# Optimization experiments

Hardware: AMD Instinct MI355X
Metric: run time of the kernel (lower is better)

## Reference

```python
import jax, jax.numpy as jnp
import numpy as np

N_HIDDEN = 15


def lstm_cell(x, h, c, W_ih, W_hh, b_ih, b_hh):
    # x: [B, in], h/c: [B, H]. PyTorch LSTMCell gate order: i, f, g, o
    gates = x @ W_ih.T + h @ W_hh.T + b_ih + b_hh  # [B, 4H]
    i, f, g, o = jnp.split(gates, 4, axis=-1)
    i = jax.nn.sigmoid(i)
    f = jax.nn.sigmoid(f)
    g = jnp.tanh(g)
    o = jax.nn.sigmoid(o)
    c_new = f * c + i * g
    h_new = o * jnp.tanh(c_new)
    return h_new, c_new


def setup_inputs() -> dict:
    key = jax.random.key(0)
    ks = jax.random.split(key, 12)
    B, T, H = 4096, 1024, N_HIDDEN
    s = 1.0 / np.sqrt(H)  # torch default init bound
    u = lambda k, shape: jax.random.uniform(k, shape, jnp.float32, -s, s)
    return {
        "input": jax.random.normal(ks[0], (B, T), jnp.float32),
        "W_ih1": u(ks[1], (4 * H, 1)),
        "W_hh1": u(ks[2], (4 * H, H)),
        "b_ih1": u(ks[3], (4 * H,)),
        "b_hh1": u(ks[4], (4 * H,)),
        "W_ih2": u(ks[5], (4 * H, H)),
        "W_hh2": u(ks[6], (4 * H, H)),
        "b_ih2": u(ks[7], (4 * H,)),
        "b_hh2": u(ks[8], (4 * H,)),
        "W_lin": u(ks[9], (1, H)),
        "b_lin": u(ks[10], (1,)),
        "future": 64,
    }


def reference(input, W_ih1, W_hh1, b_ih1, b_hh1, W_ih2, W_hh2, b_ih2, b_hh2, W_lin, b_lin, future):
    B = input.shape[0]
    H = N_HIDDEN
    zeros = jnp.zeros((B, H), input.dtype)

    def step(carry, x_t):
        h1, c1, h2, c2 = carry
        h1, c1 = lstm_cell(x_t, h1, c1, W_ih1, W_hh1, b_ih1, b_hh1)
        h2, c2 = lstm_cell(h1, h2, c2, W_ih2, W_hh2, b_ih2, b_hh2)
        out = h2 @ W_lin.T + b_lin  # [B, 1]
        return (h1, c1, h2, c2), out

    xs = input.T[:, :, None]  # [T, B, 1]
    carry, outs = jax.lax.scan(step, (zeros, zeros, zeros, zeros), xs)

    last_out = outs[-1]  # [B, 1]

    def fut_step(carry, _):
        h1, c1, h2, c2, out = carry
        (h1, c1, h2, c2), out = step((h1, c1, h2, c2), out)
        return (h1, c1, h2, c2, out), out

    _, fut_outs = jax.lax.scan(fut_step, (*carry, last_out), None, length=future)

    all_outs = jnp.concatenate([outs, fut_outs], axis=0)  # [T+future, B, 1]
    return all_outs[:, :, 0].T  # [B, T+future]
```

## Files before the change

### kernel.cpp

```cpp
#include <hip/hip_runtime.h>

#define HID   15
#define TMAIN 1024
#define FUT   64
#define OUTW  (TMAIN + FUT)

typedef _Float16 v2h __attribute__((ext_vector_type(2)));

__device__ __forceinline__ float rcp_(float x)  { return __builtin_amdgcn_rcpf(x); }
__device__ __forceinline__ float exp2_(float x) { return __builtin_amdgcn_exp2f(x); }
__device__ __forceinline__ float tanh_(float x) {
    return __builtin_fmaf(2.0f, rcp_(1.0f + exp2_(x * -2.885390081777927f)), -1.0f);
}

template<int I> struct ic { static constexpr int v = I; };
template<int J, int N, class F>
__device__ __forceinline__ void unroll_for(F&& f) {
    if constexpr (J < N) { f(ic<J>{}); unroll_for<J + 1, N>(f); }
}

template<int CTRL>
__device__ __forceinline__ int dppi(int x) {
    return __builtin_amdgcn_update_dpp(0, x, CTRL, 0xF, 0xF, true);
}
template<int CTRL>
__device__ __forceinline__ float dppf(float x) {
    return __int_as_float(dppi<CTRL>(__float_as_int(x)));
}
__device__ __forceinline__ float row_sum_bcast(float p) {
    p += dppf<0x111>(p);
    p += dppf<0x112>(p);
    p += dppf<0x114>(p);
    p += dppf<0x118>(p);
    return dppf<0x15F>(p);
}
__device__ __forceinline__ float fdot2(v2h a, v2h b, float c) {
    return __builtin_amdgcn_fdot2(a, b, c, false);
}
__device__ __forceinline__ v2h pkrtz(float lo, float hi) {
    return __builtin_bit_cast(v2h, __builtin_amdgcn_cvt_pkrtz(lo, hi));
}

__global__ __launch_bounds__(256)
__attribute__((amdgpu_waves_per_eu(1, 1)))
void lstm_seq_kernel(const float* __restrict__ input,
                     const float* __restrict__ W_ih1, const float* __restrict__ W_hh1,
                     const float* __restrict__ b_ih1, const float* __restrict__ b_hh1,
                     const float* __restrict__ W_ih2, const float* __restrict__ W_hh2,
                     const float* __restrict__ b_ih2, const float* __restrict__ b_hh2,
                     const float* __restrict__ W_lin, const float* __restrict__ b_lin,
                     float* __restrict__ out)
{
    const int tid  = threadIdx.x;
    const int wq   = tid >> 6;
    const int lane = tid & 63;
    const int g    = lane >> 4;
    const int k    = lane & 15;
    const int b0   = (blockIdx.x * 4 + wq) * 4;

    const bool pad = (k >= HID);
    const float m  = pad ? 0.0f : 1.0f;
    const int  kk  = pad ? 0 : k;

    const float L2E = 1.442695040888963f;
    const float sA[4] = {-L2E, -L2E, -2.0f * L2E, -L2E};

    v2h w1[4][8], w2i[4][8], w2h[4][8];
    float bb1[4], bb2[4];
    #pragma unroll
    for (int gi = 0; gi < 4; ++gi) {
        const int row = gi * HID + kk;
        const float s = m * sA[gi];
        bb1[gi] = s * (b_ih1[row] + b_hh1[row]);
        bb2[gi] = s * (b_ih2[row] + b_hh2[row]);
        #pragma unroll
        for (int j = 0; j < 8; ++j) {
            const int c0 = 2 * j, c1i = 2 * j + 1;
            w1 [gi][j] = (v2h){(_Float16)(s * W_hh1[row * HID + c0]),
                               (_Float16)((c1i < HID) ? s * W_hh1[row * HID + c1i]
                                                      : s * W_ih1[row])};
            w2i[gi][j] = (v2h){(_Float16)(s * W_ih2[row * HID + c0]),
                               (_Float16)((c1i < HID) ? s * W_ih2[row * HID + c1i] : 0.0f)};
            w2h[gi][j] = (v2h){(_Float16)(s * W_hh2[row * HID + c0]),
                               (_Float16)((c1i < HID) ? s * W_hh2[row * HID + c1i] : 0.0f)};
        }
    }
    const float wl   = m * W_lin[kk];
    const float blin = b_lin[0];

    auto packh = [&](float h) -> int {
        const _Float16 hh = (_Float16)h;
        const int lo = (int)(unsigned short)__builtin_bit_cast(unsigned short, hh);
        const int hi = dppi<0x101>(lo);
        const v2h pr = {__builtin_bit_cast(_Float16, (unsigned short)lo),
                        __builtin_bit_cast(_Float16, (unsigned short)(hi & 0xFFFF))};
        return __builtin_bit_cast(int, pr);
    };

    v2h hb1[8];
    #pragma unroll
    for (int j = 0; j < 8; ++j) hb1[j] = (v2h){(_Float16)0.0f, (_Float16)0.0f};
    int hpk2 = 0;
    float c1 = 0.0f, c2 = 0.0f, outv = 0.0f;

    auto step = [&](auto Sc, auto UseOvC, float xvpre, float& oreg) {
        constexpr int  S      = decltype(Sc)::v;
        constexpr bool USE_OV = decltype(UseOvC)::v;

        float a0 = bb1[0], a1 = bb1[1], a2 = bb1[2], a3 = bb1[3];
        unroll_for<0, 8>([&](auto jc) {
            constexpr int j = decltype(jc)::v;
            a0 = fdot2(w1[0][j], hb1[j], a0);
            a1 = fdot2(w1[1][j], hb1[j], a1);
            a2 = fdot2(w1[2][j], hb1[j], a2);
            a3 = fdot2(w1[3][j], hb1[j], a3);
        });

        float d0 = bb2[0], d1 = bb2[1], d2 = bb2[2], d3 = bb2[3];
        unroll_for<0, 8>([&](auto jc) {
            constexpr int j = decltype(jc)::v;
            const v2h hb = __builtin_bit_cast(v2h, dppi<0x150 + 2*j>(hpk2));
            d0 = fdot2(w2h[0][j], hb, d0);
            d1 = fdot2(w2h[1][j], hb, d1);
            d2 = fdot2(w2h[2][j], hb, d2);
            d3 = fdot2(w2h[3][j], hb, d3);
        });

        const float ig = rcp_(1.0f + exp2_(a0));
        const float fg = rcp_(1.0f + exp2_(a1));
        const float gg = __builtin_fmaf(2.0f, rcp_(1.0f + exp2_(a2)), -1.0f);
        const float og = rcp_(1.0f + exp2_(a3));
        c1 = __builtin_fmaf(fg, c1, ig * gg);
        const float h1n = og * tanh_(c1);

        const int hpk1 = packh(h1n);
        unroll_for<0, 8>([&](auto jc) {
            constexpr int j = decltype(jc)::v;
            hb1[j] = __builtin_bit_cast(v2h, dppi<0x150 + 2*j>(hpk1));
        });
        unroll_for<0, 8>([&](auto jc) {
            constexpr int j = decltype(jc)::v;
            d0 = fdot2(w2i[0][j], hb1[j], d0);
            d1 = fdot2(w2i[1][j], hb1[j], d1);
            d2 = fdot2(w2i[2][j], hb1[j], d2);
            d3 = fdot2(w2i[3][j], hb1[j], d3);
        });

        const float i2 = rcp_(1.0f + exp2_(d0));
        const float f2 = rcp_(1.0f + exp2_(d1));
        const float g2 = __builtin_fmaf(2.0f, rcp_(1.0f + exp2_(d2)), -1.0f);
        const float o2 = rcp_(1.0f + exp2_(d3));
        c2 = __builtin_fmaf(f2, c2, i2 * g2);
        const float h2n = o2 * tanh_(c2);
        hpk2 = packh(h2n);

        const float ov = row_sum_bcast(wl * h2n) + blin;
        oreg = (k == S) ? ov : oreg;

        const float xv = USE_OV ? ov : xvpre;
        hb1[7] = pkrtz(dppf<0x15E>(h1n), xv);

        outv = ov;
    };

    const size_t inb  = (size_t)(b0 + g) * TMAIN + k;
    const size_t outb = (size_t)(b0 + g) * OUTW  + k;

    float xcur = input[inb];
    hb1[7] = pkrtz(0.0f, dppf<0x150>(xcur));

    #pragma unroll 1
    for (int ch = 0; ch < TMAIN / 16; ++ch) {
        const bool last = (ch == TMAIN / 16 - 1);
        const float xnext = input[inb + (last ? ch : ch + 1) * 16];
        float oreg = 0.0f;
        unroll_for<0, 16>([&](auto sc) {
            constexpr int s = decltype(sc)::v;
            if constexpr (s < 15) {
                step(sc, ic<0>{}, dppf<0x150 + s + 1>(xcur), oreg);
            } else {
                if (last) step(sc, ic<1>{}, 0.0f, oreg);
                else      step(sc, ic<0>{}, dppf<0x150>(xnext), oreg);
            }
        });
        out[outb + ch * 16] = oreg;
        xcur = xnext;
    }

    #pragma unroll 1
    for (int ch = 0; ch < FUT / 16; ++ch) {
        float oreg = 0.0f;
        unroll_for<0, 16>([&](auto sc) {
            step(sc, ic<1>{}, 0.0f, oreg);
        });
        out[outb + TMAIN + ch * 16] = oreg;
    }
}

extern "C" void kernel_launch(void* const* d_in, const int* in_sizes, int n_in,
                              void* d_out, int out_size, void* d_ws, size_t ws_size,
                              hipStream_t stream)
{
    const float* input = (const float*)d_in[0];
    const float* W_ih1 = (const float*)d_in[1];
    const float* W_hh1 = (const float*)d_in[2];
    const float* b_ih1 = (const float*)d_in[3];
    const float* b_hh1 = (const float*)d_in[4];
    const float* W_ih2 = (const float*)d_in[5];
    const float* W_hh2 = (const float*)d_in[6];
    const float* b_ih2 = (const float*)d_in[7];
    const float* b_hh2 = (const float*)d_in[8];
    const float* W_lin = (const float*)d_in[9];
    const float* b_lin = (const float*)d_in[10];

    lstm_seq_kernel<<<256, 256, 0, stream>>>(
        input, W_ih1, W_hh1, b_ih1, b_hh1,
        W_ih2, W_hh2, b_ih2, b_hh2, W_lin, b_lin,
        (float*)d_out);
}
```

Measured before the change: 471.4 us.

## Replace per-lane fdot2 gate matvecs with MFMA 16x16x32 matrix ops

The recurrent and input gate matvecs, which were done with chains of v_dot2 instructions on DPP-broadcast hidden states, now run on MFMA 16x16x32 f16. Weights are packed into A operands with the bias folded in as an extra K column. The B operand is built from packed h via ds_bpermute, and results are redistributed to lanes with bpermute plus selects. The aim is to cut VALU dot-product work on the sequential critical path. In exchange each step pays MFMA latency and LDS-crossbar permutes, and most of the 16x16 output is wasted work.

```diff
diff --git a/kernel.cpp b/kernel.cpp
--- a/kernel.cpp
+++ b/kernel.cpp
@@ -6,6 +6,9 @@
 #define OUTW  (TMAIN + FUT)
 
 typedef _Float16 v2h __attribute__((ext_vector_type(2)));
+typedef _Float16 v8h __attribute__((ext_vector_type(8)));
+typedef float    v4f __attribute__((ext_vector_type(4)));
+typedef int      v4i __attribute__((ext_vector_type(4)));
 
 __device__ __forceinline__ float rcp_(float x)  { return __builtin_amdgcn_rcpf(x); }
 __device__ __forceinline__ float exp2_(float x) { return __builtin_amdgcn_exp2f(x); }
@@ -34,11 +37,11 @@
     p += dppf<0x118>(p);
     return dppf<0x15F>(p);
 }
-__device__ __forceinline__ float fdot2(v2h a, v2h b, float c) {
-    return __builtin_amdgcn_fdot2(a, b, c, false);
-}
-__device__ __forceinline__ v2h pkrtz(float lo, float hi) {
-    return __builtin_bit_cast(v2h, __builtin_amdgcn_cvt_pkrtz(lo, hi));
+__device__ __forceinline__ int bperm(int addr, int src) {
+    return __builtin_amdgcn_ds_bpermute(addr, src);
+}
+__device__ __forceinline__ v4f mfma16x32(v8h a, v8h b, v4f c) {
+    return __builtin_amdgcn_mfma_f32_16x16x32_f16(a, b, c, 0, 0, 0);
 }
 
 __global__ __launch_bounds__(256)
@@ -59,34 +62,51 @@
     const int b0   = (blockIdx.x * 4 + wq) * 4;
 
     const bool pad = (k >= HID);
+    const int  kk  = pad ? 0 : k;
     const float m  = pad ? 0.0f : 1.0f;
-    const int  kk  = pad ? 0 : k;
 
     const float L2E = 1.442695040888963f;
     const float sA[4] = {-L2E, -L2E, -2.0f * L2E, -L2E};
 
-    v2h w1[4][8], w2i[4][8], w2h[4][8];
-    float bb1[4], bb2[4];
+    v8h A1[4], A2[4];
     #pragma unroll
     for (int gi = 0; gi < 4; ++gi) {
         const int row = gi * HID + kk;
         const float s = m * sA[gi];
-        bb1[gi] = s * (b_ih1[row] + b_hh1[row]);
-        bb2[gi] = s * (b_ih2[row] + b_hh2[row]);
         #pragma unroll
         for (int j = 0; j < 8; ++j) {
-            const int c0 = 2 * j, c1i = 2 * j + 1;
-            w1 [gi][j] = (v2h){(_Float16)(s * W_hh1[row * HID + c0]),
-                               (_Float16)((c1i < HID) ? s * W_hh1[row * HID + c1i]
-                                                      : s * W_ih1[row])};
-            w2i[gi][j] = (v2h){(_Float16)(s * W_ih2[row * HID + c0]),
-                               (_Float16)((c1i < HID) ? s * W_ih2[row * HID + c1i] : 0.0f)};
-            w2h[gi][j] = (v2h){(_Float16)(s * W_hh2[row * HID + c0]),
-                               (_Float16)((c1i < HID) ? s * W_hh2[row * HID + c1i] : 0.0f)};
+            const int kd = g * 8 + j;
+            float a1 = 0.0f, a2 = 0.0f;
+            if (kd < HID) {
+                a1 = s * W_hh1[row * HID + kd];
+                a2 = s * W_ih2[row * HID + kd];
+            } else if (kd == HID) {
+                a1 = s * (b_ih1[row] + b_hh1[row]);
+                a2 = s * (b_ih2[row] + b_hh2[row]);
+            } else if (kd >= 16 && kd - 16 < HID) {
+                a2 = s * W_hh2[row * HID + (kd - 16)];
+            }
+            A1[gi][j] = (_Float16)a1;
+            A2[gi][j] = (_Float16)a2;
         }
     }
+
+    float wihx[4];
+    #pragma unroll
+    for (int gi = 0; gi < 4; ++gi)
+        wihx[gi] = m * sA[gi] * W_ih1[gi * HID + kk];
     const float wl   = m * W_lin[kk];
     const float blin = b_lin[0];
+
+    const int ab0 = 4 * ((lane & 15) * 16 + ((lane >> 4) & 1) * 8);
+    const int ab1 = ab0 + 8;
+    const int ab2 = ab0 + 16;
+    const int ab3 = ab0 + 24;
+    const int adD = 4 * (((lane & 15) >> 2) * 16 + (lane >> 4));
+    const bool k1   = (k & 1) != 0;
+    const bool k2   = (k & 2) != 0;
+    const bool qlow = (g < 2);
+    const int  mskb = (g == 1) ? 0x3C000000 : 0;
 
     auto packh = [&](float h) -> int {
         const _Float16 hh = (_Float16)h;
@@ -97,34 +117,55 @@
         return __builtin_bit_cast(int, pr);
     };
 
-    v2h hb1[8];
-    #pragma unroll
-    for (int j = 0; j < 8; ++j) hb1[j] = (v2h){(_Float16)0.0f, (_Float16)0.0f};
-    int hpk2 = 0;
+    auto buildB2 = [&](int pk1, int pk2) -> v8h {
+        const int t0a = bperm(ab0, pk1), t0b = bperm(ab0, pk2);
+        const int t1a = bperm(ab1, pk1), t1b = bperm(ab1, pk2);
+        const int t2a = bperm(ab2, pk1), t2b = bperm(ab2, pk2);
+        const int t3a = bperm(ab3, pk1), t3b = bperm(ab3, pk2);
+        v4i r;
+        r[0] = qlow ? t0a : t0b;
+        r[1] = qlow ? t1a : t1b;
+        r[2] = qlow ? t2a : t2b;
+        r[3] = (qlow ? t3a : t3b) | mskb;
+        return __builtin_bit_cast(v8h, r);
+    };
+    auto deriveB1 = [&](v8h b2) -> v8h {
+        v4i r = __builtin_bit_cast(v4i, b2);
+        r[0] = qlow ? r[0] : 0;
+        r[1] = qlow ? r[1] : 0;
+        r[2] = qlow ? r[2] : 0;
+        r[3] = qlow ? r[3] : 0;
+        return __builtin_bit_cast(v8h, r);
+    };
+    auto redist = [&](v4f D) -> float {
+        const int t0 = bperm(adD, __float_as_int(D[0]));
+        const int t1 = bperm(adD, __float_as_int(D[1]));
+        const int t2 = bperm(adD, __float_as_int(D[2]));
+        const int t3 = bperm(adD, __float_as_int(D[3]));
+        const int s01 = k1 ? t1 : t0;
+        const int s23 = k1 ? t3 : t2;
+        return __int_as_float(k2 ? s23 : s01);
+    };
+
+    v4i binit = {0, 0, 0, mskb};
+    v8h B1cur = __builtin_bit_cast(v8h, binit);
+    int pk2 = 0;
     float c1 = 0.0f, c2 = 0.0f, outv = 0.0f;
-
-    auto step = [&](auto Sc, auto UseOvC, float xvpre, float& oreg) {
+    const v4f z4 = {0.0f, 0.0f, 0.0f, 0.0f};
+
+    auto step = [&](auto Sc, auto UseOvC, float xbpre, float& oreg) {
         constexpr int  S      = decltype(Sc)::v;
         constexpr bool USE_OV = decltype(UseOvC)::v;
 
-        float a0 = bb1[0], a1 = bb1[1], a2 = bb1[2], a3 = bb1[3];
-        unroll_for<0, 8>([&](auto jc) {
-            constexpr int j = decltype(jc)::v;
-            a0 = fdot2(w1[0][j], hb1[j], a0);
-            a1 = fdot2(w1[1][j], hb1[j], a1);
-            a2 = fdot2(w1[2][j], hb1[j], a2);
-            a3 = fdot2(w1[3][j], hb1[j], a3);
-        });
-
-        float d0 = bb2[0], d1 = bb2[1], d2 = bb2[2], d3 = bb2[3];
-        unroll_for<0, 8>([&](auto jc) {
-            constexpr int j = decltype(jc)::v;
-            const v2h hb = __builtin_bit_cast(v2h, dppi<0x150 + 2*j>(hpk2));
-            d0 = fdot2(w2h[0][j], hb, d0);
-            d1 = fdot2(w2h[1][j], hb, d1);
-            d2 = fdot2(w2h[2][j], hb, d2);
-            d3 = fdot2(w2h[3][j], hb, d3);
-        });
+        const v4f D0 = mfma16x32(A1[0], B1cur, z4);
+        const v4f D1 = mfma16x32(A1[1], B1cur, z4);
+        const v4f D2 = mfma16x32(A1[2], B1cur, z4);
+        const v4f D3 = mfma16x32(A1[3], B1cur, z4);
+        const float xb = USE_OV ? outv : xbpre;
+        const float a0 = __builtin_fmaf(wihx[0], xb, redist(D0));
+        const float a1 = __builtin_fmaf(wihx[1], xb, redist(D1));
+        const float a2 = __builtin_fmaf(wihx[2], xb, redist(D2));
+        const float a3 = __builtin_fmaf(wihx[3], xb, redist(D3));
 
         const float ig = rcp_(1.0f + exp2_(a0));
         const float fg = rcp_(1.0f + exp2_(a1));
@@ -133,18 +174,16 @@
         c1 = __builtin_fmaf(fg, c1, ig * gg);
         const float h1n = og * tanh_(c1);
 
-        const int hpk1 = packh(h1n);
-        unroll_for<0, 8>([&](auto jc) {
-            constexpr int j = decltype(jc)::v;
-            hb1[j] = __builtin_bit_cast(v2h, dppi<0x150 + 2*j>(hpk1));
-        });
-        unroll_for<0, 8>([&](auto jc) {
-            constexpr int j = decltype(jc)::v;
-            d0 = fdot2(w2i[0][j], hb1[j], d0);
-            d1 = fdot2(w2i[1][j], hb1[j], d1);
-            d2 = fdot2(w2i[2][j], hb1[j], d2);
-            d3 = fdot2(w2i[3][j], hb1[j], d3);
-        });
+        const int pk1 = packh(h1n);
+        const v8h B2  = buildB2(pk1, pk2);
+        const v4f E0 = mfma16x32(A2[0], B2, z4);
+        const v4f E1 = mfma16x32(A2[1], B2, z4);
+        const v4f E2 = mfma16x32(A2[2], B2, z4);
+        const v4f E3 = mfma16x32(A2[3], B2, z4);
+        const float d0 = redist(E0);
+        const float d1 = redist(E1);
+        const float d2 = redist(E2);
+        const float d3 = redist(E3);
 
         const float i2 = rcp_(1.0f + exp2_(d0));
         const float f2 = rcp_(1.0f + exp2_(d1));
@@ -152,39 +191,29 @@
         const float o2 = rcp_(1.0f + exp2_(d3));
         c2 = __builtin_fmaf(f2, c2, i2 * g2);
         const float h2n = o2 * tanh_(c2);
-        hpk2 = packh(h2n);
+        pk2 = packh(h2n);
+        B1cur = deriveB1(B2);
 
         const float ov = row_sum_bcast(wl * h2n) + blin;
         oreg = (k == S) ? ov : oreg;
-
-        const float xv = USE_OV ? ov : xvpre;
-        hb1[7] = pkrtz(dppf<0x15E>(h1n), xv);
-
         outv = ov;
     };
 
     const size_t inb  = (size_t)(b0 + g) * TMAIN + k;
     const size_t outb = (size_t)(b0 + g) * OUTW  + k;
 
-    float xcur = input[inb];
-    hb1[7] = pkrtz(0.0f, dppf<0x150>(xcur));
-
+    float xnext = input[inb];
     #pragma unroll 1
     for (int ch = 0; ch < TMAIN / 16; ++ch) {
-        const bool last = (ch == TMAIN / 16 - 1);
-        const float xnext = input[inb + (last ? ch : ch + 1) * 16];
+        const float xcur = xnext;
+        const int tn = (ch < TMAIN / 16 - 1) ? (ch + 1) * 16 : ch * 16;
+        xnext = input[inb + tn];
         float oreg = 0.0f;
         unroll_for<0, 16>([&](auto sc) {
             constexpr int s = decltype(sc)::v;
-            if constexpr (s < 15) {
-                step(sc, ic<0>{}, dppf<0x150 + s + 1>(xcur), oreg);
-            } else {
-                if (last) step(sc, ic<1>{}, 0.0f, oreg);
-                else      step(sc, ic<0>{}, dppf<0x150>(xnext), oreg);
-            }
+            step(sc, ic<0>{}, dppf<0x150 + s>(xcur), oreg);
         });
         out[outb + ch * 16] = oreg;
-        xcur = xnext;
     }
 
     #pragma unroll 1
```

After: 713.2 us. 51.3% more time.
